# Kernel optimization log

Measured on AMD Instinct MI355X. Metric: run time of the kernel, lower is better.

The kernel has to match this reference:

```python
import jax, jax.numpy as jnp
import numpy as np

NEG_SLOPE = 0.2  # PyG GATConv default leaky_relu slope
EPS = 1e-16      # PyG softmax denominator eps


def gat_conv(x, edge_index, W, b, att_src, att_dst, heads, ch, concat):
    """Faithful PyG GATConv (eval mode, self-loops already in edge_index).
    x: [N, F_in]; W: [F_in, heads*ch]; att_src/att_dst: [1, heads, ch]; b: [out]."""
    N = x.shape[0]
    h = (x @ W).reshape(N, heads, ch)                      # [N, H, C]
    a_s = jnp.sum(h * att_src, axis=-1)                    # [N, H]
    a_d = jnp.sum(h * att_dst, axis=-1)                    # [N, H]
    src, dst = edge_index[0], edge_index[1]
    alpha = jax.nn.leaky_relu(a_s[src] + a_d[dst], NEG_SLOPE)  # [E, H]
    # segment softmax over edges grouped by destination node
    amax = jax.ops.segment_max(alpha, dst, num_segments=N)     # [N, H]
    amax = jnp.where(jnp.isfinite(amax), amax, 0.0)
    ex = jnp.exp(alpha - amax[dst])                            # [E, H]
    denom = jax.ops.segment_sum(ex, dst, num_segments=N)       # [N, H]
    alpha = ex / (denom[dst] + EPS)
    msg = alpha[:, :, None] * h[src]                           # [E, H, C]
    out = jax.ops.segment_sum(msg, dst, num_segments=N)        # [N, H, C]
    out = out.reshape(N, heads * ch) if concat else out.mean(axis=1)
    return out + b


def setup_inputs() -> dict:
    key = jax.random.key(0)
    ks = jax.random.split(key, 10)
    N, E, F_in, num_classes = 100000, 1600000, 128, 16
    H1, C1 = 8, 8
    x = jax.random.normal(ks[0], (N, F_in), dtype=jnp.float32)
    edge_index = jax.random.randint(ks[1], (2, E), 0, N, dtype=jnp.int64)
    s1 = (2.0 / (F_in + H1 * C1)) ** 0.5
    W1 = jax.random.normal(ks[2], (F_in, H1 * C1), dtype=jnp.float32) * s1
    b1 = jnp.zeros((H1 * C1,), dtype=jnp.float32)
    att_src1 = jax.random.normal(ks[3], (1, H1, C1), dtype=jnp.float32) * 0.3
    att_dst1 = jax.random.normal(ks[4], (1, H1, C1), dtype=jnp.float32) * 0.3
    s2 = (2.0 / (H1 * C1 + num_classes)) ** 0.5
    W2 = jax.random.normal(ks[5], (H1 * C1, num_classes), dtype=jnp.float32) * s2
    b2 = jnp.zeros((num_classes,), dtype=jnp.float32)
    att_src2 = jax.random.normal(ks[6], (1, 1, num_classes), dtype=jnp.float32) * 0.3
    att_dst2 = jax.random.normal(ks[7], (1, 1, num_classes), dtype=jnp.float32) * 0.3
    return {"x": x, "edge_index": edge_index, "W1": W1, "b1": b1,
            "att_src1": att_src1, "att_dst1": att_dst1,
            "W2": W2, "b2": b2, "att_src2": att_src2, "att_dst2": att_dst2}


def reference(x, edge_index, W1, b1, att_src1, att_dst1, W2, b2, att_src2, att_dst2):
    N = x.shape[0]
    # PyG default add_self_loops=True in both GATConv layers
    loops = jnp.arange(N, dtype=edge_index.dtype)
    ei = jnp.concatenate([edge_index, jnp.stack([loops, loops])], axis=1)
    h = gat_conv(x, ei, W1, b1, att_src1, att_dst1, heads=8, ch=8, concat=True)
    h = jax.nn.elu(h)
    out = gat_conv(h, ei, W2, b2, att_src2, att_dst2, heads=1, ch=16, concat=True)
    return jax.nn.log_softmax(out, axis=1)
```

## Files before the change

kernel.cpp:

```cpp
#include <hip/hip_runtime.h>
#include <hip/hip_bf16.h>


#define NEG_SLOPE 0.2f
#define EPS_DEN 1e-16f
#define CSHIFT 8.0f
#define NBUCK_MAX 256
#define BCAP 16384
#define ECHUNK 2048
#define G1_PITCH 136

typedef __attribute__((ext_vector_type(8))) short bf16x8;
typedef __attribute__((ext_vector_type(4))) float f32x4;

__device__ __forceinline__ float bf2f(unsigned short u) {
    return __uint_as_float(((unsigned)u) << 16);
}
__device__ __forceinline__ unsigned short f2bf(float f) {
    unsigned x = __float_as_uint(f);
    unsigned r = x + 0x7fffu + ((x >> 16) & 1u);
    return (unsigned short)(r >> 16);
}


__global__ __launch_bounds__(256) void bucket_kernel(
    const int* __restrict__ src, const int* __restrict__ dst,
    int* __restrict__ gcur, int* __restrict__ buf, int E, int nbuck)
{
    __shared__ int cnt[NBUCK_MAX];
    __shared__ int offs[NBUCK_MAX];
    int tid = threadIdx.x;
    for (int i = tid; i < nbuck; i += 256) cnt[i] = 0;
    __syncthreads();
    int base = blockIdx.x * ECHUNK;
    int lim = min(base + ECHUNK, E);
    int dl[8];
#pragma unroll
    for (int k = 0; k < 8; ++k) {
        int e = base + tid + 256 * k;
        dl[k] = (e < lim) ? dst[e] : -1;
    }
#pragma unroll
    for (int k = 0; k < 8; ++k)
        if (dl[k] >= 0) atomicAdd(&cnt[dl[k] >> 9], 1);
    __syncthreads();
    for (int i = tid; i < nbuck; i += 256) {
        offs[i] = atomicAdd(&gcur[i], cnt[i]);
        cnt[i] = 0;
    }
    __syncthreads();
#pragma unroll
    for (int k = 0; k < 8; ++k) {
        if (dl[k] >= 0) {
            int e = base + tid + 256 * k;
            int b = dl[k] >> 9;
            int idx = offs[b] + atomicAdd(&cnt[b], 1);
            if (idx < BCAP)
                buf[(size_t)b * BCAP + idx] = (src[e] << 9) | (dl[k] & 511);
        }
    }
}

__global__ void gscan_kernel(const int* __restrict__ gcur, int* __restrict__ gbase, int B) {
    int lane = threadIdx.x;
    int carry = 0;
    for (int base = 0; base < B; base += 64) {
        int i = base + lane;
        int v = (i < B) ? gcur[i] : 0;
        int sc = v;
#pragma unroll
        for (int off = 1; off < 64; off <<= 1) {
            int o = __shfl_up(sc, off);
            if (lane >= off) sc += o;
        }
        if (i < B) gbase[i] = carry + sc - v;
        carry += __shfl(sc, 63);
    }
}

__global__ __launch_bounds__(256) void csr_bucket_kernel(
    const int* __restrict__ gcur, const int* __restrict__ gbase,
    const int* __restrict__ buf, int* __restrict__ rowptr,
    int* __restrict__ srcs, int N, int E)
{
    __shared__ int cnt[512];
    __shared__ int wsum[4];
    __shared__ int wbase[4];
    int b = blockIdx.x, tid = threadIdx.x;
    int lane = tid & 63, wv = tid >> 6;
    cnt[2 * tid] = 0; cnt[2 * tid + 1] = 0;
    __syncthreads();
    int n = min(gcur[b], BCAP);
    const int* p = buf + (size_t)b * BCAP;
    for (int i = tid; i < n; i += 256) atomicAdd(&cnt[p[i] & 511], 1);
    __syncthreads();
    int c0 = cnt[2 * tid], c1 = cnt[2 * tid + 1];
    int s = c0 + c1;
    int sc = s;
#pragma unroll
    for (int off = 1; off < 64; off <<= 1) {
        int o = __shfl_up(sc, off);
        if (lane >= off) sc += o;
    }
    if (lane == 63) wsum[wv] = sc;
    __syncthreads();
    if (tid == 0) {
        int acc = 0;
#pragma unroll
        for (int k = 0; k < 4; ++k) { wbase[k] = acc; acc += wsum[k]; }
    }
    __syncthreads();
    int base = gbase[b];
    int g0 = base + wbase[wv] + (sc - s);
    int g1 = g0 + c0;
    int node0 = (b << 9) + 2 * tid;
    if (node0 < N)     rowptr[node0]     = g0;
    if (node0 + 1 < N) rowptr[node0 + 1] = g1;
    cnt[2 * tid] = g0; cnt[2 * tid + 1] = g1;
    __syncthreads();
    for (int i = tid; i < n; i += 256) {
        int v = p[i];
        int posi = atomicAdd(&cnt[v & 511], 1);
        srcs[posi] = v >> 9;
    }
    if (b == 0 && tid == 0) rowptr[N] = E;
}


__global__ __launch_bounds__(256) void gemm1_mfma_kernel(
    const float* __restrict__ x, const float* __restrict__ W1,
    const float* __restrict__ att_s, const float* __restrict__ att_d,
    unsigned short* __restrict__ h1b, float* __restrict__ a_s,
    float* __restrict__ a_d, int N)
{
    __shared__ unsigned short As[64 * G1_PITCH];
    __shared__ unsigned short Cs[64 * 68];
    int tid = threadIdx.x;
    int lane = tid & 63, wv = tid >> 6;
    int quad = lane >> 4, l16 = lane & 15;

    bf16x8 Bf[4][4];
#pragma unroll
    for (int ks = 0; ks < 4; ++ks)
#pragma unroll
        for (int nt = 0; nt < 4; ++nt) {
            bf16x8 f;
#pragma unroll
            for (int j = 0; j < 8; ++j)
                f[j] = (short)f2bf(W1[(ks * 32 + quad * 8 + j) * 64 + nt * 16 + l16]);
            Bf[ks][nt] = f;
        }
    float asw[4], adw[4];
#pragma unroll
    for (int nt = 0; nt < 4; ++nt) {
        asw[nt] = att_s[nt * 16 + l16];
        adw[nt] = att_d[nt * 16 + l16];
    }

    int nblocks = (N + 63) >> 6;
    for (int blk = blockIdx.x; blk < nblocks; blk += gridDim.x) {
        int row0 = blk << 6;
        __syncthreads();
#pragma unroll
        for (int i = 0; i < 8; ++i) {
            int idx = tid + 256 * i;
            int r = idx >> 5, c4 = idx & 31;
            int row = row0 + r;
            float4 v = (row < N) ? ((const float4*)x)[(size_t)row * 32 + c4]
                                 : make_float4(0.f, 0.f, 0.f, 0.f);
            ushort4 u;
            u.x = f2bf(v.x); u.y = f2bf(v.y); u.z = f2bf(v.z); u.w = f2bf(v.w);
            *(ushort4*)&As[r * G1_PITCH + c4 * 4] = u;
        }
        __syncthreads();
        f32x4 acc[4];
#pragma unroll
        for (int nt = 0; nt < 4; ++nt) acc[nt] = (f32x4){0.f, 0.f, 0.f, 0.f};
#pragma unroll
        for (int ks = 0; ks < 4; ++ks) {
            bf16x8 Af = *(const bf16x8*)&As[(wv * 16 + l16) * G1_PITCH + ks * 32 + quad * 8];
#pragma unroll
            for (int nt = 0; nt < 4; ++nt)
                acc[nt] = __builtin_amdgcn_mfma_f32_16x16x32_bf16(Af, Bf[ks][nt], acc[nt], 0, 0, 0);
        }
        int lrow = wv * 16 + quad * 4;
#pragma unroll
        for (int nt = 0; nt < 4; ++nt) {
            float ps[4], pd[4];
#pragma unroll
            for (int r = 0; r < 4; ++r) {
                ps[r] = acc[nt][r] * asw[nt];
                pd[r] = acc[nt][r] * adw[nt];
            }
#pragma unroll
            for (int off = 1; off < 8; off <<= 1)
#pragma unroll
                for (int r = 0; r < 4; ++r) {
                    ps[r] += __shfl_xor(ps[r], off);
                    pd[r] += __shfl_xor(pd[r], off);
                }
            if ((l16 & 7) == 0) {
                int head = nt * 2 + (l16 >> 3);
#pragma unroll
                for (int r = 0; r < 4; ++r) {
                    int row = row0 + lrow + r;
                    if (row < N) {
                        a_s[row * 8 + head] = ps[r];
                        a_d[row * 8 + head] = pd[r];
                    }
                }
            }
        }
#pragma unroll
        for (int nt = 0; nt < 4; ++nt)
#pragma unroll
            for (int r = 0; r < 4; ++r)
                Cs[(lrow + r) * 68 + nt * 16 + l16] = f2bf(acc[nt][r]);
        __syncthreads();
#pragma unroll
        for (int i = 0; i < 4; ++i) {
            int idx = tid + 256 * i;
            int r = idx >> 4, c4 = idx & 15;
            int row = row0 + r;
            if (row < N) {
                ushort4 u = *(const ushort4*)&Cs[r * 68 + c4 * 4];
                ((ushort4*)h1b)[(size_t)row * 16 + c4] = u;
            }
        }
    }
}


__global__ __launch_bounds__(256) void agg1_kernel(
    const unsigned short* __restrict__ h1b, const float* __restrict__ a_s,
    const float* __restrict__ a_d, const int* __restrict__ rowptr,
    const int* __restrict__ srcs, const float* __restrict__ b1,
    unsigned short* __restrict__ heb, int N)
{
    int lane = threadIdx.x & 63, wid = threadIdx.x >> 6;
    int node = blockIdx.x * 4 + wid;
    if (node >= N) return;
    int q = lane >> 4, pos = lane & 15, hp = pos >> 1;
    int beg = rowptr[node], end = rowptr[node + 1];
    float adn = a_d[node * 8 + hp];
    const ushort4* h1v = (const ushort4*)h1b;

    float l = 0.f, a0 = 0.f, a1 = 0.f, a2 = 0.f, a3 = 0.f;
    if (q == 0) {
        float v = a_s[node * 8 + hp] + adn;
        v = fmaxf(v, NEG_SLOPE * v);
        float p = __expf(v - CSHIFT);
        ushort4 h = h1v[(size_t)node * 16 + pos];
        l = p;
        a0 = p * bf2f(h.x); a1 = p * bf2f(h.y);
        a2 = p * bf2f(h.z); a3 = p * bf2f(h.w);
    }
    int e = beg + q;
    for (; e + 12 < end; e += 16) {
        int s0 = srcs[e], s1 = srcs[e + 4], s2 = srcs[e + 8], s3 = srcs[e + 12];
        float va0 = a_s[s0 * 8 + hp], va1 = a_s[s1 * 8 + hp];
        float va2 = a_s[s2 * 8 + hp], va3 = a_s[s3 * 8 + hp];
        ushort4 h0 = h1v[(size_t)s0 * 16 + pos];
        ushort4 h1_ = h1v[(size_t)s1 * 16 + pos];
        ushort4 h2_ = h1v[(size_t)s2 * 16 + pos];
        ushort4 h3_ = h1v[(size_t)s3 * 16 + pos];
        float v0 = va0 + adn; v0 = fmaxf(v0, NEG_SLOPE * v0);
        float v1 = va1 + adn; v1 = fmaxf(v1, NEG_SLOPE * v1);
        float v2 = va2 + adn; v2 = fmaxf(v2, NEG_SLOPE * v2);
        float v3 = va3 + adn; v3 = fmaxf(v3, NEG_SLOPE * v3);
        float p0 = __expf(v0 - CSHIFT), p1 = __expf(v1 - CSHIFT);
        float p2 = __expf(v2 - CSHIFT), p3 = __expf(v3 - CSHIFT);
        l += p0 + p1 + p2 + p3;
        a0 = fmaf(p0, bf2f(h0.x), a0); a1 = fmaf(p0, bf2f(h0.y), a1);
        a2 = fmaf(p0, bf2f(h0.z), a2); a3 = fmaf(p0, bf2f(h0.w), a3);
        a0 = fmaf(p1, bf2f(h1_.x), a0); a1 = fmaf(p1, bf2f(h1_.y), a1);
        a2 = fmaf(p1, bf2f(h1_.z), a2); a3 = fmaf(p1, bf2f(h1_.w), a3);
        a0 = fmaf(p2, bf2f(h2_.x), a0); a1 = fmaf(p2, bf2f(h2_.y), a1);
        a2 = fmaf(p2, bf2f(h2_.z), a2); a3 = fmaf(p2, bf2f(h2_.w), a3);
        a0 = fmaf(p3, bf2f(h3_.x), a0); a1 = fmaf(p3, bf2f(h3_.y), a1);
        a2 = fmaf(p3, bf2f(h3_.z), a2); a3 = fmaf(p3, bf2f(h3_.w), a3);
    }
    for (; e < end; e += 4) {
        int s = srcs[e];
        float va = a_s[s * 8 + hp];
        ushort4 h = h1v[(size_t)s * 16 + pos];
        float v = va + adn; v = fmaxf(v, NEG_SLOPE * v);
        float p = __expf(v - CSHIFT);
        l += p;
        a0 = fmaf(p, bf2f(h.x), a0); a1 = fmaf(p, bf2f(h.y), a1);
        a2 = fmaf(p, bf2f(h.z), a2); a3 = fmaf(p, bf2f(h.w), a3);
    }
#pragma unroll
    for (int off = 16; off < 64; off <<= 1) {
        l  += __shfl_xor(l, off);
        a0 += __shfl_xor(a0, off); a1 += __shfl_xor(a1, off);
        a2 += __shfl_xor(a2, off); a3 += __shfl_xor(a3, off);
    }
    if (q == 0) {
        float inv = 1.f / (l + EPS_DEN);
        float4 bb = ((const float4*)b1)[pos];
        float o0 = fmaf(a0, inv, bb.x);
        float o1 = fmaf(a1, inv, bb.y);
        float o2 = fmaf(a2, inv, bb.z);
        float o3 = fmaf(a3, inv, bb.w);
        o0 = o0 > 0.f ? o0 : __expf(o0) - 1.f;
        o1 = o1 > 0.f ? o1 : __expf(o1) - 1.f;
        o2 = o2 > 0.f ? o2 : __expf(o2) - 1.f;
        o3 = o3 > 0.f ? o3 : __expf(o3) - 1.f;
        ushort4 u;
        u.x = f2bf(o0); u.y = f2bf(o1); u.z = f2bf(o2); u.w = f2bf(o3);
        ((ushort4*)heb)[(size_t)node * 16 + pos] = u;
    }
}


__global__ __launch_bounds__(256) void gemm2_kernel(
    const unsigned short* __restrict__ heb, const float* __restrict__ W2,
    const float* __restrict__ att_s2, const float* __restrict__ att_d2,
    unsigned short* __restrict__ h2b, float* __restrict__ a_s2,
    float* __restrict__ a_d2, int N)
{
    __shared__ float xs[4][4 * 68];
    int lane = threadIdx.x & 63, wid = threadIdx.x >> 6;
    int sub = lane >> 4, c = lane & 15;
    float wcol[64];
#pragma unroll
    for (int k = 0; k < 64; ++k) wcol[k] = W2[k * 16 + c];
    float asw = att_s2[c], adw = att_d2[c];
    int groups = (N + 15) >> 4;
    int iters = (groups + gridDim.x - 1) / gridDim.x;
    for (int it = 0; it < iters; ++it) {
        int g = blockIdx.x + it * gridDim.x;
        int nb = g * 16 + wid * 4;
        __syncthreads();
        if (g < groups) {
#pragma unroll
            for (int i = 0; i < 4; ++i) {
                int n = nb + i;
                xs[wid][i * 68 + lane] = (n < N) ? bf2f(heb[(size_t)n * 64 + lane]) : 0.f;
            }
        }
        __syncthreads();
        if (g < groups) {
            int node = nb + sub;
            const float4* xv = (const float4*)&xs[wid][sub * 68];
            float acc = 0.f;
#pragma unroll
            for (int k4 = 0; k4 < 16; ++k4) {
                float4 v = xv[k4];
                acc += v.x * wcol[4 * k4 + 0] + v.y * wcol[4 * k4 + 1]
                     + v.z * wcol[4 * k4 + 2] + v.w * wcol[4 * k4 + 3];
            }
            if (node < N) {
                h2b[(size_t)node * 16 + c] = f2bf(acc);
                float rs = acc * asw, rd = acc * adw;
#pragma unroll
                for (int off = 1; off < 16; off <<= 1) {
                    rs += __shfl_xor(rs, off);
                    rd += __shfl_xor(rd, off);
                }
                if (c == 0) { a_s2[node] = rs; a_d2[node] = rd; }
            }
        }
    }
}


__global__ __launch_bounds__(256) void agg2_kernel(
    const unsigned short* __restrict__ h2b, const float* __restrict__ a_s2,
    const float* __restrict__ a_d2, const int* __restrict__ rowptr,
    const int* __restrict__ srcs, const float* __restrict__ b2,
    float* __restrict__ out, int N)
{
    int lane = threadIdx.x & 63, wid = threadIdx.x >> 6;
    int node = blockIdx.x * 4 + wid;
    if (node >= N) return;
    int q = lane >> 2, pos = lane & 3;
    int beg = rowptr[node], end = rowptr[node + 1];
    float adn = a_d2[node];
    const ushort4* h2v = (const ushort4*)h2b;

    float l = 0.f, a0 = 0.f, a1 = 0.f, a2 = 0.f, a3 = 0.f;
    if (q == 0) {
        float v = a_s2[node] + adn;
        v = fmaxf(v, NEG_SLOPE * v);
        float p = __expf(v - CSHIFT);
        ushort4 h = h2v[(size_t)node * 4 + pos];
        l = p;
        a0 = p * bf2f(h.x); a1 = p * bf2f(h.y);
        a2 = p * bf2f(h.z); a3 = p * bf2f(h.w);
    }
    int e = beg + q;
    for (; e + 16 < end; e += 32) {
        int s0 = srcs[e], s1 = srcs[e + 16];
        float va0 = a_s2[s0], va1 = a_s2[s1];
        ushort4 h0 = h2v[(size_t)s0 * 4 + pos];
        ushort4 h1_ = h2v[(size_t)s1 * 4 + pos];
        float v0 = va0 + adn; v0 = fmaxf(v0, NEG_SLOPE * v0);
        float v1 = va1 + adn; v1 = fmaxf(v1, NEG_SLOPE * v1);
        float p0 = __expf(v0 - CSHIFT), p1 = __expf(v1 - CSHIFT);
        l += p0 + p1;
        a0 = fmaf(p0, bf2f(h0.x), a0); a1 = fmaf(p0, bf2f(h0.y), a1);
        a2 = fmaf(p0, bf2f(h0.z), a2); a3 = fmaf(p0, bf2f(h0.w), a3);
        a0 = fmaf(p1, bf2f(h1_.x), a0); a1 = fmaf(p1, bf2f(h1_.y), a1);
        a2 = fmaf(p1, bf2f(h1_.z), a2); a3 = fmaf(p1, bf2f(h1_.w), a3);
    }
    for (; e < end; e += 16) {
        int s = srcs[e];
        float va = a_s2[s];
        ushort4 h = h2v[(size_t)s * 4 + pos];
        float v = va + adn; v = fmaxf(v, NEG_SLOPE * v);
        float p = __expf(v - CSHIFT);
        l += p;
        a0 = fmaf(p, bf2f(h.x), a0); a1 = fmaf(p, bf2f(h.y), a1);
        a2 = fmaf(p, bf2f(h.z), a2); a3 = fmaf(p, bf2f(h.w), a3);
    }
#pragma unroll
    for (int off = 4; off < 64; off <<= 1) {
        l  += __shfl_xor(l, off);
        a0 += __shfl_xor(a0, off); a1 += __shfl_xor(a1, off);
        a2 += __shfl_xor(a2, off); a3 += __shfl_xor(a3, off);
    }
    if (q == 0) {
        float inv = 1.f / (l + EPS_DEN);
        float4 bb = ((const float4*)b2)[pos];
        float o0 = fmaf(a0, inv, bb.x);
        float o1 = fmaf(a1, inv, bb.y);
        float o2 = fmaf(a2, inv, bb.z);
        float o3 = fmaf(a3, inv, bb.w);
        float mx = fmaxf(fmaxf(o0, o1), fmaxf(o2, o3));
        mx = fmaxf(mx, __shfl_xor(mx, 1));
        mx = fmaxf(mx, __shfl_xor(mx, 2));
        float se = __expf(o0 - mx) + __expf(o1 - mx)
                 + __expf(o2 - mx) + __expf(o3 - mx);
        se += __shfl_xor(se, 1);
        se += __shfl_xor(se, 2);
        float ls = mx + logf(se);
        ((float4*)out)[(size_t)node * 4 + pos] =
            make_float4(o0 - ls, o1 - ls, o2 - ls, o3 - ls);
    }
}


extern "C" void kernel_launch(void* const* d_in, const int* in_sizes, int n_in,
                              void* d_out, int out_size, void* d_ws, size_t ws_size,
                              hipStream_t stream) {
    const float* x    = (const float*)d_in[0];
    const int*   ei   = (const int*)d_in[1];
    const float* W1   = (const float*)d_in[2];
    const float* b1   = (const float*)d_in[3];
    const float* as1  = (const float*)d_in[4];
    const float* ad1  = (const float*)d_in[5];
    const float* W2   = (const float*)d_in[6];
    const float* b2   = (const float*)d_in[7];
    const float* as2  = (const float*)d_in[8];
    const float* ad2  = (const float*)d_in[9];
    float* out = (float*)d_out;

    int N = in_sizes[0] / 128;
    int E = in_sizes[1] / 2;
    const int* srcp = ei;
    const int* dstp = ei + E;
    int nbuck = (N + 511) >> 9;

    char* w = (char*)d_ws;
    auto alloc = [&](size_t bytes) {
        void* p = (void*)w;
        w += (bytes + 255) & ~(size_t)255;
        return p;
    };
    unsigned short* h1b = (unsigned short*)alloc((size_t)N * 64 * 2);
    float* a_s1  = (float*)alloc((size_t)N * 8 * 4);
    float* a_d1  = (float*)alloc((size_t)N * 8 * 4);
    unsigned short* heb = (unsigned short*)alloc((size_t)N * 64 * 2);
    unsigned short* h2b = (unsigned short*)alloc((size_t)N * 16 * 2);
    float* a_s2b = (float*)alloc((size_t)N * 4);
    float* a_d2b = (float*)alloc((size_t)N * 4);
    int*   rowp  = (int*)alloc((size_t)(N + 1) * 4);
    int*   srcs  = (int*)alloc((size_t)E * 4);
    int*   gcur  = (int*)alloc((size_t)nbuck * 4);
    int*   gbase = (int*)alloc((size_t)nbuck * 4);
    int*   buf   = (int*)alloc((size_t)nbuck * BCAP * 4);

    hipMemsetAsync(gcur, 0, (size_t)nbuck * 4, stream);

    int bblk = (E + ECHUNK - 1) / ECHUNK;
    bucket_kernel<<<bblk, 256, 0, stream>>>(srcp, dstp, gcur, buf, E, nbuck);
    gscan_kernel<<<1, 64, 0, stream>>>(gcur, gbase, nbuck);
    csr_bucket_kernel<<<nbuck, 256, 0, stream>>>(gcur, gbase, buf, rowp, srcs, N, E);

    int g1blocks = (N + 63) >> 6;
    gemm1_mfma_kernel<<<g1blocks, 256, 0, stream>>>(x, W1, as1, ad1, h1b, a_s1, a_d1, N);
    agg1_kernel<<<(N + 3) / 4, 256, 0, stream>>>(h1b, a_s1, a_d1, rowp, srcs, b1, heb, N);
    gemm2_kernel<<<512, 256, 0, stream>>>(heb, W2, as2, ad2, h2b, a_s2b, a_d2b, N);
    agg2_kernel<<<(N + 3) / 4, 256, 0, stream>>>(h2b, a_s2b, a_d2b, rowp, srcs, b2, out, N);
}
```

Baseline: 296.1 us.

## Fuse layer-2 projection into layer-1 aggregation and fold bucket scan into CSR

```diff
diff --git a/kernel.cpp b/kernel.cpp
--- a/kernel.cpp
+++ b/kernel.cpp
@@ -61,34 +61,24 @@
     }
 }
 
-__global__ void gscan_kernel(const int* __restrict__ gcur, int* __restrict__ gbase, int B) {
-    int lane = threadIdx.x;
-    int carry = 0;
-    for (int base = 0; base < B; base += 64) {
-        int i = base + lane;
-        int v = (i < B) ? gcur[i] : 0;
-        int sc = v;
-#pragma unroll
-        for (int off = 1; off < 64; off <<= 1) {
-            int o = __shfl_up(sc, off);
-            if (lane >= off) sc += o;
-        }
-        if (i < B) gbase[i] = carry + sc - v;
-        carry += __shfl(sc, 63);
-    }
-}
-
 __global__ __launch_bounds__(256) void csr_bucket_kernel(
-    const int* __restrict__ gcur, const int* __restrict__ gbase,
-    const int* __restrict__ buf, int* __restrict__ rowptr,
-    int* __restrict__ srcs, int N, int E)
+    const int* __restrict__ gcur, const int* __restrict__ buf,
+    int* __restrict__ rowptr, int* __restrict__ srcs, int N, int E)
 {
     __shared__ int cnt[512];
     __shared__ int wsum[4];
     __shared__ int wbase[4];
+    __shared__ int basesh;
     int b = blockIdx.x, tid = threadIdx.x;
     int lane = tid & 63, wv = tid >> 6;
     cnt[2 * tid] = 0; cnt[2 * tid + 1] = 0;
+    int part = 0;
+    for (int i = tid; i < b; i += 256) part += gcur[i];
+#pragma unroll
+    for (int off = 32; off >= 1; off >>= 1) part += __shfl_xor(part, off);
+    if (lane == 0) wsum[wv] = part;
+    __syncthreads();
+    if (tid == 0) basesh = wsum[0] + wsum[1] + wsum[2] + wsum[3];
     __syncthreads();
     int n = min(gcur[b], BCAP);
     const int* p = buf + (size_t)b * BCAP;
@@ -110,8 +100,7 @@
         for (int k = 0; k < 4; ++k) { wbase[k] = acc; acc += wsum[k]; }
     }
     __syncthreads();
-    int base = gbase[b];
-    int g0 = base + wbase[wv] + (sc - s);
+    int g0 = basesh + wbase[wv] + (sc - s);
     int g1 = g0 + c0;
     int node0 = (b << 9) + 2 * tid;
     if (node0 < N)     rowptr[node0]     = g0;
@@ -231,11 +220,13 @@
 }
 
 
-__global__ __launch_bounds__(256) void agg1_kernel(
+__global__ __launch_bounds__(256) void agg1_fused_kernel(
     const unsigned short* __restrict__ h1b, const float* __restrict__ a_s,
     const float* __restrict__ a_d, const int* __restrict__ rowptr,
     const int* __restrict__ srcs, const float* __restrict__ b1,
-    unsigned short* __restrict__ heb, int N)
+    const float* __restrict__ W2, const float* __restrict__ att_s2,
+    const float* __restrict__ att_d2, unsigned short* __restrict__ h2b,
+    float* __restrict__ a_s2, float* __restrict__ a_d2, int N)
 {
     int lane = threadIdx.x & 63, wid = threadIdx.x >> 6;
     int node = blockIdx.x * 4 + wid;
@@ -296,73 +287,41 @@
         a0 += __shfl_xor(a0, off); a1 += __shfl_xor(a1, off);
         a2 += __shfl_xor(a2, off); a3 += __shfl_xor(a3, off);
     }
-    if (q == 0) {
-        float inv = 1.f / (l + EPS_DEN);
-        float4 bb = ((const float4*)b1)[pos];
-        float o0 = fmaf(a0, inv, bb.x);
-        float o1 = fmaf(a1, inv, bb.y);
-        float o2 = fmaf(a2, inv, bb.z);
-        float o3 = fmaf(a3, inv, bb.w);
-        o0 = o0 > 0.f ? o0 : __expf(o0) - 1.f;
-        o1 = o1 > 0.f ? o1 : __expf(o1) - 1.f;
-        o2 = o2 > 0.f ? o2 : __expf(o2) - 1.f;
-        o3 = o3 > 0.f ? o3 : __expf(o3) - 1.f;
+    float inv = 1.f / (l + EPS_DEN);
+    float4 bb = ((const float4*)b1)[pos];
+    float o0 = fmaf(a0, inv, bb.x);
+    float o1 = fmaf(a1, inv, bb.y);
+    float o2 = fmaf(a2, inv, bb.z);
+    float o3 = fmaf(a3, inv, bb.w);
+    o0 = o0 > 0.f ? o0 : __expf(o0) - 1.f;
+    o1 = o1 > 0.f ? o1 : __expf(o1) - 1.f;
+    o2 = o2 > 0.f ? o2 : __expf(o2) - 1.f;
+    o3 = o3 > 0.f ? o3 : __expf(o3) - 1.f;
+    float4 w0 = *(const float4*)(W2 + (4 * pos + 0) * 16 + 4 * q);
+    float4 w1 = *(const float4*)(W2 + (4 * pos + 1) * 16 + 4 * q);
+    float4 w2 = *(const float4*)(W2 + (4 * pos + 2) * 16 + 4 * q);
+    float4 w3 = *(const float4*)(W2 + (4 * pos + 3) * 16 + 4 * q);
+    float r0 = o0 * w0.x + o1 * w1.x + o2 * w2.x + o3 * w3.x;
+    float r1 = o0 * w0.y + o1 * w1.y + o2 * w2.y + o3 * w3.y;
+    float r2 = o0 * w0.z + o1 * w1.z + o2 * w2.z + o3 * w3.z;
+    float r3 = o0 * w0.w + o1 * w1.w + o2 * w2.w + o3 * w3.w;
+#pragma unroll
+    for (int off = 1; off < 16; off <<= 1) {
+        r0 += __shfl_xor(r0, off); r1 += __shfl_xor(r1, off);
+        r2 += __shfl_xor(r2, off); r3 += __shfl_xor(r3, off);
+    }
+    float4 ws = ((const float4*)att_s2)[q];
+    float4 wd = ((const float4*)att_d2)[q];
+    float ps = r0 * ws.x + r1 * ws.y + r2 * ws.z + r3 * ws.w;
+    float pd = r0 * wd.x + r1 * wd.y + r2 * wd.z + r3 * wd.w;
+    ps += __shfl_xor(ps, 16); pd += __shfl_xor(pd, 16);
+    ps += __shfl_xor(ps, 32); pd += __shfl_xor(pd, 32);
+    if (pos == 0) {
         ushort4 u;
-        u.x = f2bf(o0); u.y = f2bf(o1); u.z = f2bf(o2); u.w = f2bf(o3);
-        ((ushort4*)heb)[(size_t)node * 16 + pos] = u;
-    }
-}
-
-
-__global__ __launch_bounds__(256) void gemm2_kernel(
-    const unsigned short* __restrict__ heb, const float* __restrict__ W2,
-    const float* __restrict__ att_s2, const float* __restrict__ att_d2,
-    unsigned short* __restrict__ h2b, float* __restrict__ a_s2,
-    float* __restrict__ a_d2, int N)
-{
-    __shared__ float xs[4][4 * 68];
-    int lane = threadIdx.x & 63, wid = threadIdx.x >> 6;
-    int sub = lane >> 4, c = lane & 15;
-    float wcol[64];
-#pragma unroll
-    for (int k = 0; k < 64; ++k) wcol[k] = W2[k * 16 + c];
-    float asw = att_s2[c], adw = att_d2[c];
-    int groups = (N + 15) >> 4;
-    int iters = (groups + gridDim.x - 1) / gridDim.x;
-    for (int it = 0; it < iters; ++it) {
-        int g = blockIdx.x + it * gridDim.x;
-        int nb = g * 16 + wid * 4;
-        __syncthreads();
-        if (g < groups) {
-#pragma unroll
-            for (int i = 0; i < 4; ++i) {
-                int n = nb + i;
-                xs[wid][i * 68 + lane] = (n < N) ? bf2f(heb[(size_t)n * 64 + lane]) : 0.f;
-            }
-        }
-        __syncthreads();
-        if (g < groups) {
-            int node = nb + sub;
-            const float4* xv = (const float4*)&xs[wid][sub * 68];
-            float acc = 0.f;
-#pragma unroll
-            for (int k4 = 0; k4 < 16; ++k4) {
-                float4 v = xv[k4];
-                acc += v.x * wcol[4 * k4 + 0] + v.y * wcol[4 * k4 + 1]
-                     + v.z * wcol[4 * k4 + 2] + v.w * wcol[4 * k4 + 3];
-            }
-            if (node < N) {
-                h2b[(size_t)node * 16 + c] = f2bf(acc);
-                float rs = acc * asw, rd = acc * adw;
-#pragma unroll
-                for (int off = 1; off < 16; off <<= 1) {
-                    rs += __shfl_xor(rs, off);
-                    rd += __shfl_xor(rd, off);
-                }
-                if (c == 0) { a_s2[node] = rs; a_d2[node] = rd; }
-            }
-        }
-    }
+        u.x = f2bf(r0); u.y = f2bf(r1); u.z = f2bf(r2); u.w = f2bf(r3);
+        ((ushort4*)h2b)[(size_t)node * 4 + q] = u;
+    }
+    if (lane == 0) { a_s2[node] = ps; a_d2[node] = pd; }
 }
 
 
@@ -472,26 +431,23 @@
     unsigned short* h1b = (unsigned short*)alloc((size_t)N * 64 * 2);
     float* a_s1  = (float*)alloc((size_t)N * 8 * 4);
     float* a_d1  = (float*)alloc((size_t)N * 8 * 4);
-    unsigned short* heb = (unsigned short*)alloc((size_t)N * 64 * 2);
     unsigned short* h2b = (unsigned short*)alloc((size_t)N * 16 * 2);
     float* a_s2b = (float*)alloc((size_t)N * 4);
     float* a_d2b = (float*)alloc((size_t)N * 4);
     int*   rowp  = (int*)alloc((size_t)(N + 1) * 4);
     int*   srcs  = (int*)alloc((size_t)E * 4);
     int*   gcur  = (int*)alloc((size_t)nbuck * 4);
-    int*   gbase = (int*)alloc((size_t)nbuck * 4);
     int*   buf   = (int*)alloc((size_t)nbuck * BCAP * 4);
 
     hipMemsetAsync(gcur, 0, (size_t)nbuck * 4, stream);
 
     int bblk = (E + ECHUNK - 1) / ECHUNK;
     bucket_kernel<<<bblk, 256, 0, stream>>>(srcp, dstp, gcur, buf, E, nbuck);
-    gscan_kernel<<<1, 64, 0, stream>>>(gcur, gbase, nbuck);
-    csr_bucket_kernel<<<nbuck, 256, 0, stream>>>(gcur, gbase, buf, rowp, srcs, N, E);
+    csr_bucket_kernel<<<nbuck, 256, 0, stream>>>(gcur, buf, rowp, srcs, N, E);
 
     int g1blocks = (N + 63) >> 6;
     gemm1_mfma_kernel<<<g1blocks, 256, 0, stream>>>(x, W1, as1, ad1, h1b, a_s1, a_d1, N);
-    agg1_kernel<<<(N + 3) / 4, 256, 0, stream>>>(h1b, a_s1, a_d1, rowp, srcs, b1, heb, N);
-    gemm2_kernel<<<512, 256, 0, stream>>>(heb, W2, as2, ad2, h2b, a_s2b, a_d2b, N);
+    agg1_fused_kernel<<<(N + 3) / 4, 256, 0, stream>>>(
+        h1b, a_s1, a_d1, rowp, srcs, b1, W2, as2, ad2, h2b, a_s2b, a_d2b, N);
     agg2_kernel<<<(N + 3) / 4, 256, 0, stream>>>(h2b, a_s2b, a_d2b, rowp, srcs, b2, out, N);
 }
```

Measured after the change: 303.6 us. +2.5%, slower.
